# Performance work log

Measured on AMD Instinct MI355X. Metric: run time of the kernel, lower is better.

Reference implementation:

```python
import jax, jax.numpy as jnp
import numpy as np

THRESHOLD = 0.99
B, M, H = 8, 2048, 1024


def setup_inputs():
    key = jax.random.key(0)
    ks = jax.random.split(key, 8)
    x = jax.random.normal(ks[0], (B, M, H), jnp.float32)
    run = jax.random.randint(ks[1], (B, M), 0, 2) > 0
    acc_p = jax.random.uniform(ks[2], (B, M, 1), jnp.float32) * 0.6
    weighted_h = jax.random.normal(ks[3], (B, M, H), jnp.float32)
    remainders = jnp.zeros((B, M, 1), jnp.float32)
    exit_ = jnp.zeros((B, M, 1), jnp.int32)
    pad_h = jax.random.normal(ks[4], (H,), jnp.float32)
    p_w = jax.random.normal(ks[5], (H, 1), jnp.float32) / np.sqrt(H)
    p_b = jnp.zeros((1,), jnp.float32)
    return {"x": x, "run": run, "acc_p": acc_p, "weighted_h": weighted_h,
            "remainders": remainders, "exit_": exit_, "updates": 3,
            "pad_h": pad_h, "p_w": p_w, "p_b": p_b}


def _unpack(x, run):
    # restore left-packed x to full [B, M, H] with zeros at non-run slots
    rank = jnp.cumsum(run, axis=1) - 1                      # [B, M] position in packed row
    g = jnp.take_along_axis(x, jnp.maximum(rank, 0)[..., None], axis=1)
    return jnp.where(run[..., None], g, jnp.zeros((), x.dtype))


def _pack(h, run, pad_h):
    # left-pack run tokens; tail slots get the pad vector (pad_ semantics).
    # Static-shape variant of torch pack: output is [B, M, H] (max_ <= M).
    order = jnp.argsort(~run, axis=1)                       # stable sort: run tokens first
    packed = jnp.take_along_axis(h, order[..., None], axis=1)
    counts = jnp.sum(run, axis=1, keepdims=True)            # [B, 1]
    valid = jnp.arange(run.shape[1])[None, :] < counts      # [B, M]
    return jnp.where(valid[..., None], packed, pad_h[None, None, :])


def reference(x, run, acc_p, weighted_h, remainders, exit_, updates, pad_h, p_w, p_b):
    runf = run[..., None].astype(x.dtype)                   # [B, M, 1]
    h = _unpack(x, run)                                     # [B, M, H]
    p = jax.nn.sigmoid(jnp.einsum('bmh,ho->bmo', h, p_w) + p_b) * runf
    mask_continue = ((acc_p + p) < THRESHOLD) & run[..., None]
    mask_exit = (~mask_continue) & run[..., None]
    mc = mask_continue.astype(x.dtype)
    me = mask_exit.astype(x.dtype)
    update = p * mc + (1.0 - acc_p) * me
    weighted_h_new = h * update + weighted_h
    run_new = run & mask_continue[..., 0]
    acc_p_new = acc_p + update * mc
    remainders_new = remainders + (1.0 - acc_p_new) * me
    updates_new = updates + 1
    exit_new = exit_ + updates_new * mask_exit.astype(exit_.dtype)
    h_packed = _pack(h, run_new, pad_h)
    return (h_packed, weighted_h_new, acc_p_new, remainders_new, run_new, exit_new)
```

## Files before the change

### kernel.cpp

```cpp
#include <hip/hip_runtime.h>

#define BB 8
#define MM 2048
#define HH 1024
#define THRESH 0.99f
#define BMH ((size_t)BB * MM * HH)
#define BM (BB * MM)
#define CHUNK 16
#define CPR (MM / CHUNK)
#define NBLK (BM / CHUNK)
#define RDY 0x40000000

typedef float f32x4 __attribute__((ext_vector_type(4)));

__device__ inline f32x4 ntload4(const float* p) {
    return __builtin_nontemporal_load((const f32x4*)p);
}
__device__ inline void ntstore4(float* p, f32x4 v) {
    __builtin_nontemporal_store(v, (f32x4*)p);
}
__device__ inline f32x4 ld4(const float* p) { return *(const f32x4*)p; }

__global__ __launch_bounds__(256, 4) void act_kernel(
    const float* __restrict__ x, const int* __restrict__ run,
    const float* __restrict__ acc_p, const float* __restrict__ weighted_h,
    const float* __restrict__ remainders, const int* __restrict__ exit_,
    const int* __restrict__ updates, const float* __restrict__ pad_h,
    const float* __restrict__ p_w, const float* __restrict__ p_b,
    float* __restrict__ out_hpacked, float* __restrict__ out_wh,
    float* __restrict__ out_accp, float* __restrict__ out_rem,
    float* __restrict__ out_run, float* __restrict__ out_exit,
    int* __restrict__ mask_ws) {
    __shared__ int wsum[4];
    __shared__ int cflag[CHUNK], cnew[CHUNK], crank[CHUNK], crank2[CHUNK];
    __shared__ int rowmask[CPR];

    const int chunk = blockIdx.x;
    const int t0  = chunk * CHUNK;
    const int b   = t0 >> 11;
    const int m0  = t0 & (MM - 1);
    const int myc = chunk & (CPR - 1);
    const int* rrow = run + b * MM;
    const int tid  = threadIdx.x;
    const int wave = tid >> 6;
    const int lane = tid & 63;

    f32x4 wv[4];
#pragma unroll
    for (int j = 0; j < 4; ++j) wv[j] = ld4(p_w + j * 256 + lane * 4);

    int s = 0;
    for (int i = tid; i < m0; i += 256) s += (rrow[i] != 0) ? 1 : 0;
#pragma unroll
    for (int off = 32; off > 0; off >>= 1) s += __shfl_xor(s, off, 64);
    if (lane == 0) wsum[wave] = s;
    if (tid < CHUNK) cflag[tid] = (rrow[m0 + tid] != 0) ? 1 : 0;
    __syncthreads();
    const int base0 = wsum[0] + wsum[1] + wsum[2] + wsum[3];
    if (tid < CHUNK) {
        int r = base0;
#pragma unroll
        for (int i = 0; i < CHUNK; ++i) r += (i <= tid) ? cflag[i] : 0;
        crank[tid] = r - 1;
    }
    __syncthreads();

    const float pb = p_b[0];
    const int upd1 = updates[0] + 1;
#pragma unroll
    for (int q = 0; q < 4; ++q) {
        const int ti = wave * 4 + q;
        const int t  = t0 + ti;
        const bool r = (cflag[ti] != 0);
        f32x4 hv[4];
        float dot = 0.f;
        if (r) {
            const float* xrow = x + ((size_t)(b * MM + crank[ti])) * HH;
#pragma unroll
            for (int j = 0; j < 4; ++j) {
                const int idx = j * 256 + lane * 4;
                hv[j] = ld4(xrow + idx);
                dot += hv[j].x * wv[j].x + hv[j].y * wv[j].y +
                       hv[j].z * wv[j].z + hv[j].w * wv[j].w;
            }
        } else {
#pragma unroll
            for (int j = 0; j < 4; ++j) hv[j] = (f32x4)(0.f);
        }
#pragma unroll
        for (int off = 32; off > 0; off >>= 1) dot += __shfl_xor(dot, off, 64);

        const float p = r ? (1.f / (1.f + expf(-(dot + pb)))) : 0.f;
        const float ap = acc_p[t];
        const bool mc = r && ((ap + p) < THRESH);
        const bool me = r && !mc;
        const float upd = mc ? p : (me ? (1.f - ap) : 0.f);
        const float ap_new = mc ? (ap + p) : ap;

        const float* whrow = weighted_h + (size_t)t * HH;
        float* orow = out_wh + (size_t)t * HH;
#pragma unroll
        for (int j = 0; j < 4; ++j) {
            const int idx = j * 256 + lane * 4;
            const f32x4 w4 = ntload4(whrow + idx);
            ntstore4(orow + idx, hv[j] * upd + w4);
        }
        if (lane == 0) {
            out_accp[t] = ap_new;
            out_rem[t]  = remainders[t] + (me ? (1.f - ap_new) : 0.f);
            out_run[t]  = mc ? 1.f : 0.f;
            out_exit[t] = (float)(exit_[t] + (me ? upd1 : 0));
            cnew[ti] = mc ? 1 : 0;
        }
    }
    __syncthreads();

    if (tid == 0) {
        int m16 = 0;
#pragma unroll
        for (int i = 0; i < CHUNK; ++i) m16 |= cnew[i] << i;
        __hip_atomic_store(mask_ws + chunk, RDY | m16, __ATOMIC_RELAXED,
                           __HIP_MEMORY_SCOPE_AGENT);
    }

    if (tid < CPR) {
        const int* src = mask_ws + b * CPR + tid;
        int v;
        while (((v = __hip_atomic_load(src, __ATOMIC_RELAXED,
                                       __HIP_MEMORY_SCOPE_AGENT)) & RDY) == 0) {
            __builtin_amdgcn_s_sleep(4);
        }
        rowmask[tid] = v & 0xFFFF;
    }
    __syncthreads();

    int baseN = 0, cnt = 0;
    for (int c = 0; c < CPR; ++c) {
        const int pc = __popc(rowmask[c]);
        cnt += pc;
        baseN += (c < myc) ? pc : 0;
    }
    if (tid < CHUNK) {
        int n = baseN;
#pragma unroll
        for (int i = 0; i < CHUNK; ++i) n += (i <= tid) ? cnew[i] : 0;
        crank2[tid] = n - 1;
    }
    __syncthreads();

    f32x4 pv[4];
#pragma unroll
    for (int j = 0; j < 4; ++j) pv[j] = ld4(pad_h + j * 256 + lane * 4);

#pragma unroll
    for (int q = 0; q < 4; ++q) {
        const int ti = wave * 4 + q;
        const int t  = t0 + ti;
        const int m  = m0 + ti;
        if (cnew[ti] != 0) {
            const float* src = x + ((size_t)(b * MM + crank[ti])) * HH;
            float* dst = out_hpacked + ((size_t)(b * MM + crank2[ti])) * HH;
#pragma unroll
            for (int j = 0; j < 4; ++j) {
                const int idx = j * 256 + lane * 4;
                ntstore4(dst + idx, ld4(src + idx));
            }
        }
        if (m >= cnt) {
            float* prow = out_hpacked + (size_t)t * HH;
#pragma unroll
            for (int j = 0; j < 4; ++j) {
                const int idx = j * 256 + lane * 4;
                ntstore4(prow + idx, pv[j]);
            }
        }
    }
}

extern "C" void kernel_launch(void* const* d_in, const int* in_sizes, int n_in,
                              void* d_out, int out_size, void* d_ws, size_t ws_size,
                              hipStream_t stream) {
    const float* x          = (const float*)d_in[0];
    const int*   run        = (const int*)d_in[1];
    const float* acc_p      = (const float*)d_in[2];
    const float* weighted_h = (const float*)d_in[3];
    const float* remainders = (const float*)d_in[4];
    const int*   exit_      = (const int*)d_in[5];
    const int*   updates    = (const int*)d_in[6];
    const float* pad_h      = (const float*)d_in[7];
    const float* p_w        = (const float*)d_in[8];
    const float* p_b        = (const float*)d_in[9];

    float* out = (float*)d_out;
    float* out_hpacked = out;
    float* out_wh      = out + BMH;
    float* out_accp    = out + 2 * BMH;
    float* out_rem     = out_accp + BM;
    float* out_run     = out_rem + BM;
    float* out_exit    = out_run + BM;

    int* mask_ws = (int*)d_ws;

    hipMemsetAsync(mask_ws, 0, NBLK * sizeof(int), stream);

    act_kernel<<<NBLK, 256, 0, stream>>>(x, run, acc_p, weighted_h, remainders,
                                         exit_, updates, pad_h, p_w, p_b,
                                         out_hpacked, out_wh, out_accp, out_rem,
                                         out_run, out_exit, mask_ws);
}
```

Measured before the change: 57.31 us.

## Halve chunk size and move weighted_h update after mask publish

Shrinks each block to 8 tokens, doubling the block count and raising the occupancy hint to 8. The weighted_h read-modify-write is moved after the mask is published, so its memory traffic overlaps the wait for other blocks' masks. The prefix scan over the run row now uses int4 loads, and the row-wide mask popcount uses a wave shuffle reduction instead of a serial loop. The cost is re-reading x rows in the second phase and more blocks spinning on the cross-block flag; the spin wait relies on every block of a row being resident at once, so deadlock risk rises with more blocks.

```diff
diff --git a/kernel.cpp b/kernel.cpp
--- a/kernel.cpp
+++ b/kernel.cpp
@@ -1,15 +1,14 @@
 #include <hip/hip_runtime.h>
 
-#define BB 8
 #define MM 2048
 #define HH 1024
 #define THRESH 0.99f
-#define BMH ((size_t)BB * MM * HH)
-#define BM (BB * MM)
-#define CHUNK 16
+#define BMH ((size_t)8 * MM * HH)
+#define BM (8 * MM)
+#define CHUNK 8
+#define NBLK (BM / CHUNK)
 #define CPR (MM / CHUNK)
-#define NBLK (BM / CHUNK)
-#define RDY 0x40000000
+#define RDY 0x100
 
 typedef float f32x4 __attribute__((ext_vector_type(4)));
 
@@ -21,7 +20,7 @@
 }
 __device__ inline f32x4 ld4(const float* p) { return *(const f32x4*)p; }
 
-__global__ __launch_bounds__(256, 4) void act_kernel(
+__global__ __launch_bounds__(256, 8) void act_kernel(
     const float* __restrict__ x, const int* __restrict__ run,
     const float* __restrict__ acc_p, const float* __restrict__ weighted_h,
     const float* __restrict__ remainders, const int* __restrict__ exit_,
@@ -32,7 +31,8 @@
     float* __restrict__ out_run, float* __restrict__ out_exit,
     int* __restrict__ mask_ws) {
     __shared__ int wsum[4];
-    __shared__ int cflag[CHUNK], cnew[CHUNK], crank[CHUNK], crank2[CHUNK];
+    __shared__ int wsump[4], wsuma[4];
+    __shared__ int cflag[CHUNK], crank[CHUNK], cnew[CHUNK];
     __shared__ int rowmask[CPR];
 
     const int chunk = blockIdx.x;
@@ -45,12 +45,13 @@
     const int wave = tid >> 6;
     const int lane = tid & 63;
 
-    f32x4 wv[4];
-#pragma unroll
-    for (int j = 0; j < 4; ++j) wv[j] = ld4(p_w + j * 256 + lane * 4);
-
     int s = 0;
-    for (int i = tid; i < m0; i += 256) s += (rrow[i] != 0) ? 1 : 0;
+    const int n4 = m0 >> 2;
+    const int4* rrow4 = (const int4*)rrow;
+    for (int i = tid; i < n4; i += 256) {
+        const int4 v = rrow4[i];
+        s += (v.x != 0) + (v.y != 0) + (v.z != 0) + (v.w != 0);
+    }
 #pragma unroll
     for (int off = 32; off > 0; off >>= 1) s += __shfl_xor(s, off, 64);
     if (lane == 0) wsum[wave] = s;
@@ -67,25 +68,22 @@
 
     const float pb = p_b[0];
     const int upd1 = updates[0] + 1;
-#pragma unroll
-    for (int q = 0; q < 4; ++q) {
-        const int ti = wave * 4 + q;
+    float updv[2];
+#pragma unroll
+    for (int q = 0; q < 2; ++q) {
+        const int ti = wave * 2 + q;
         const int t  = t0 + ti;
         const bool r = (cflag[ti] != 0);
-        f32x4 hv[4];
         float dot = 0.f;
         if (r) {
             const float* xrow = x + ((size_t)(b * MM + crank[ti])) * HH;
 #pragma unroll
             for (int j = 0; j < 4; ++j) {
                 const int idx = j * 256 + lane * 4;
-                hv[j] = ld4(xrow + idx);
-                dot += hv[j].x * wv[j].x + hv[j].y * wv[j].y +
-                       hv[j].z * wv[j].z + hv[j].w * wv[j].w;
+                const f32x4 hv = ld4(xrow + idx);
+                const f32x4 wv = ld4(p_w + idx);
+                dot += hv.x * wv.x + hv.y * wv.y + hv.z * wv.z + hv.w * wv.w;
             }
-        } else {
-#pragma unroll
-            for (int j = 0; j < 4; ++j) hv[j] = (f32x4)(0.f);
         }
 #pragma unroll
         for (int off = 32; off > 0; off >>= 1) dot += __shfl_xor(dot, off, 64);
@@ -94,17 +92,8 @@
         const float ap = acc_p[t];
         const bool mc = r && ((ap + p) < THRESH);
         const bool me = r && !mc;
-        const float upd = mc ? p : (me ? (1.f - ap) : 0.f);
+        updv[q] = mc ? p : (me ? (1.f - ap) : 0.f);
         const float ap_new = mc ? (ap + p) : ap;
-
-        const float* whrow = weighted_h + (size_t)t * HH;
-        float* orow = out_wh + (size_t)t * HH;
-#pragma unroll
-        for (int j = 0; j < 4; ++j) {
-            const int idx = j * 256 + lane * 4;
-            const f32x4 w4 = ntload4(whrow + idx);
-            ntstore4(orow + idx, hv[j] * upd + w4);
-        }
         if (lane == 0) {
             out_accp[t] = ap_new;
             out_rem[t]  = remainders[t] + (me ? (1.f - ap_new) : 0.f);
@@ -116,50 +105,66 @@
     __syncthreads();
 
     if (tid == 0) {
-        int m16 = 0;
-#pragma unroll
-        for (int i = 0; i < CHUNK; ++i) m16 |= cnew[i] << i;
-        __hip_atomic_store(mask_ws + chunk, RDY | m16, __ATOMIC_RELAXED,
+        int m8 = 0;
+#pragma unroll
+        for (int i = 0; i < CHUNK; ++i) m8 |= cnew[i] << i;
+        __hip_atomic_store(mask_ws + chunk, RDY | m8, __ATOMIC_RELAXED,
                            __HIP_MEMORY_SCOPE_AGENT);
     }
 
-    if (tid < CPR) {
-        const int* src = mask_ws + b * CPR + tid;
+#pragma unroll
+    for (int q = 0; q < 2; ++q) {
+        const int ti = wave * 2 + q;
+        const int t  = t0 + ti;
+        const bool r = (cflag[ti] != 0);
+        const float upd = updv[q];
+        const float* xrow = x + ((size_t)(b * MM + crank[ti])) * HH;
+        const float* whrow = weighted_h + (size_t)t * HH;
+        float* orow = out_wh + (size_t)t * HH;
+#pragma unroll
+        for (int j = 0; j < 4; ++j) {
+            const int idx = j * 256 + lane * 4;
+            const f32x4 w4 = ntload4(whrow + idx);
+            f32x4 hv = (f32x4)(0.f);
+            if (r) hv = ld4(xrow + idx);
+            ntstore4(orow + idx, hv * upd + w4);
+        }
+    }
+
+    {
+        const int* srcp = mask_ws + b * CPR + tid;
         int v;
-        while (((v = __hip_atomic_load(src, __ATOMIC_RELAXED,
+        while (((v = __hip_atomic_load(srcp, __ATOMIC_RELAXED,
                                        __HIP_MEMORY_SCOPE_AGENT)) & RDY) == 0) {
-            __builtin_amdgcn_s_sleep(4);
-        }
-        rowmask[tid] = v & 0xFFFF;
-    }
-    __syncthreads();
-
-    int baseN = 0, cnt = 0;
-    for (int c = 0; c < CPR; ++c) {
-        const int pc = __popc(rowmask[c]);
-        cnt += pc;
-        baseN += (c < myc) ? pc : 0;
-    }
-    if (tid < CHUNK) {
-        int n = baseN;
-#pragma unroll
-        for (int i = 0; i < CHUNK; ++i) n += (i <= tid) ? cnew[i] : 0;
-        crank2[tid] = n - 1;
-    }
-    __syncthreads();
-
-    f32x4 pv[4];
-#pragma unroll
-    for (int j = 0; j < 4; ++j) pv[j] = ld4(pad_h + j * 256 + lane * 4);
-
-#pragma unroll
-    for (int q = 0; q < 4; ++q) {
-        const int ti = wave * 4 + q;
+            __builtin_amdgcn_s_sleep(2);
+        }
+        rowmask[tid] = v & 0xFF;
+    }
+    __syncthreads();
+
+    const int pc = __popc(rowmask[tid]);
+    int sp = (tid < myc) ? pc : 0;
+    int sa = pc;
+#pragma unroll
+    for (int off = 32; off > 0; off >>= 1) {
+        sp += __shfl_xor(sp, off, 64);
+        sa += __shfl_xor(sa, off, 64);
+    }
+    if (lane == 0) { wsump[wave] = sp; wsuma[wave] = sa; }
+    __syncthreads();
+    const int baseN = wsump[0] + wsump[1] + wsump[2] + wsump[3];
+    const int cnt   = wsuma[0] + wsuma[1] + wsuma[2] + wsuma[3];
+    const int mybits = rowmask[myc];
+
+#pragma unroll
+    for (int q = 0; q < 2; ++q) {
+        const int ti = wave * 2 + q;
         const int t  = t0 + ti;
         const int m  = m0 + ti;
-        if (cnew[ti] != 0) {
+        if ((mybits >> ti) & 1) {
+            const int dstrow = baseN + __popc(mybits & ((1 << (ti + 1)) - 1)) - 1;
             const float* src = x + ((size_t)(b * MM + crank[ti])) * HH;
-            float* dst = out_hpacked + ((size_t)(b * MM + crank2[ti])) * HH;
+            float* dst = out_hpacked + ((size_t)(b * MM + dstrow)) * HH;
 #pragma unroll
             for (int j = 0; j < 4; ++j) {
                 const int idx = j * 256 + lane * 4;
@@ -171,7 +176,7 @@
 #pragma unroll
             for (int j = 0; j < 4; ++j) {
                 const int idx = j * 256 + lane * 4;
-                ntstore4(prow + idx, pv[j]);
+                ntstore4(prow + idx, ld4(pad_h + idx));
             }
         }
     }
```

Measured after the change: 58.94 us. 2.8% more time.
